# Performance work log

Hardware: AMD Instinct MI355X
Metric: run time of the kernel (lower is better)

Reference implementation:

```python
import jax, jax.numpy as jnp
import numpy as np

B, N, K = 2, 16384, 8
NH, HD, CH, KV_IN = 4, 32, 128, 128
EPS = 1e-5

def layer_norm(x, g, b):
    mu = x.mean(-1, keepdims=True)
    var = ((x - mu) ** 2).mean(-1, keepdims=True)
    return (x - mu) / jnp.sqrt(var + EPS) * g + b

def setup_inputs() -> dict:
    key = jax.random.key(0)
    ks = jax.random.split(key, 8)
    s = 0.02
    return {
        "query_in": jax.random.normal(ks[0], (B, N, CH), jnp.float32),
        "kv_in": jax.random.normal(ks[1], (B, N, K, KV_IN), jnp.float32),
        "w_kv": jax.random.normal(ks[2], (KV_IN, 2 * NH * HD), jnp.float32) * s,
        "w_q": jax.random.normal(ks[3], (CH, NH * HD), jnp.float32) * s,
        "w_mh": jax.random.normal(ks[4], (NH * HD, CH), jnp.float32) * s,
        "b_mh": jnp.zeros((CH,), jnp.float32),
        "w1": jax.random.normal(ks[5], (CH, CH), jnp.float32) * s,
        "b1": jnp.zeros((CH,), jnp.float32),
        "w2": jax.random.normal(ks[6], (CH, CH), jnp.float32) * s,
        "b2": jnp.zeros((CH,), jnp.float32),
        "ln1_g": jnp.ones((CH,), jnp.float32),
        "ln1_b": jnp.zeros((CH,), jnp.float32),
        "ln2_g": jnp.ones((CH,), jnp.float32),
        "ln2_b": jnp.zeros((CH,), jnp.float32),
    }

def reference(query_in, kv_in, w_kv, w_q, w_mh, b_mh, w1, b1, w2, b2,
              ln1_g, ln1_b, ln2_g, ln2_b):
    # q projection: [B,N,CH] -> [B,N,NH,HD]
    q = (query_in @ w_q).reshape(B, N, NH, HD)
    # kv projection: [B,N,K,KV_IN] -> [B,N,K,2,NH,HD]; chunk(2) on last dim
    kv = (kv_in @ w_kv).reshape(B, N, K, 2, NH, HD)
    k, v = kv[..., 0, :, :], kv[..., 1, :, :]  # each [B,N,K,NH,HD]
    # per-token local attention over its own K keys
    sim = jnp.einsum('bnhd,bnkhd->bnhk', q, k) / np.sqrt(HD).astype(np.float32)
    attn = jax.nn.softmax(sim, axis=-1)
    out = jnp.einsum('bnhk,bnkhd->bnhd', attn, v).reshape(B, N, NH * HD)
    out = out @ w_mh + b_mh
    res = layer_norm(out, ln1_g, ln1_b) + query_in
    # GELU MLP (torch nn.GELU default = exact erf form)
    mlp = jax.nn.gelu(res @ w1 + b1, approximate=False) @ w2 + b2
    return layer_norm(mlp + res, ln2_g, ln2_b)
```

## Files before the change

### kernel.cpp

```cpp
#include <hip/hip_runtime.h>
#include <hip/hip_fp16.h>

typedef _Float16 f16x8 __attribute__((ext_vector_type(8)));
typedef float f32x4 __attribute__((ext_vector_type(4)));
typedef unsigned int uint32;

#define LDW 136
#define TB  16

#define WAITLGKM() do { __builtin_amdgcn_s_waitcnt(0xC07F); __builtin_amdgcn_sched_barrier(0); } while(0)

#define BAR() do {                                          \
  asm volatile("s_waitcnt lgkmcnt(0)" ::: "memory");        \
  __builtin_amdgcn_sched_barrier(0);                        \
  __builtin_amdgcn_s_barrier();                             \
  __builtin_amdgcn_sched_barrier(0);                        \
} while (0)

union F16x8U { f16x8 v; __half2 h2[4]; uint2 u2[2]; uint4 u4; };

__device__ __forceinline__ uint32 pk2f(float a, float b) {
  __half2 h = __floats2half2_rn(a, b);
  return *reinterpret_cast<uint32*>(&h);
}
__device__ __forceinline__ float bcast(float v, int sl) {
  return __int_as_float(__builtin_amdgcn_readlane(__float_as_int(v), sl));
}
template <int CTRL, int RMASK = 0xF, int BMASK = 0xF>
__device__ __forceinline__ float dppmov(float v) {
  return __int_as_float(__builtin_amdgcn_update_dpp(
      0, __float_as_int(v), CTRL, RMASK, BMASK, true));
}
template <int PAT>
__device__ __forceinline__ float swzf(float v) {
  return __int_as_float(__builtin_amdgcn_ds_swizzle(__float_as_int(v), PAT));
}
__device__ __forceinline__ float wred_sum(float v) {
  v += dppmov<0x111>(v);
  v += dppmov<0x112>(v);
  v += dppmov<0x114>(v);
  v += dppmov<0x118>(v);
  v += dppmov<0x142, 0xA>(v);
  v += dppmov<0x143, 0xC>(v);
  return __int_as_float(__builtin_amdgcn_readlane(__float_as_int(v), 63));
}
__device__ __forceinline__ f16x8 ldsv8(const __half* p) {
  return *reinterpret_cast<const f16x8*>(p);
}
__device__ __forceinline__ f32x4 mfma16(f16x8 a, f16x8 b, f32x4 c) {
  return __builtin_amdgcn_mfma_f32_16x16x32_f16(a, b, c, 0, 0, 0);
}
__device__ __forceinline__ void stp(__half* base, int fr, int fq, int nt, f32x4 a) {
  uint2 u; u.x = pk2f(a[0], a[1]); u.y = pk2f(a[2], a[3]);
  *reinterpret_cast<uint2*>(&base[fr * LDW + nt * 16 + fq * 4]) = u;
}

#define OFF_WQ   0
#define OFF_WK2  16384
#define OFF_WV   36864
#define OFF_WMH  53248
#define OFF_W1   69632
#define OFF_W2   86016
#define WS_HALVES 102400

__global__ void prep_weights(const float* __restrict__ wq, const float* __restrict__ wkv,
                             const float* __restrict__ wmh, const float* __restrict__ w1,
                             const float* __restrict__ w2, __half* __restrict__ ws) {
  int idx = blockIdx.x * 256 + threadIdx.x;
  if (idx >= WS_HALVES) return;
  float v;
  if (idx < OFF_WK2) {
    int t = idx, c = t >> 7, k = t & 127;
    v = wq[k * 128 + c];
  } else if (idx < OFF_WV) {
    int t = idx - OFF_WK2;
    int d = t % 40, row = t / 40;
    int h = row >> 7, i = row & 127;
    v = (d < 32) ? wkv[i * 256 + h * 32 + d] : 0.f;
  } else if (idx < OFF_WMH) {
    int t = idx - OFF_WV, c = t >> 7, k = t & 127;
    v = wkv[k * 256 + 128 + c];
  } else if (idx < OFF_W1) {
    int t = idx - OFF_WMH, c = t >> 7, k = t & 127;
    v = wmh[k * 128 + c];
  } else if (idx < OFF_W2) {
    int t = idx - OFF_W1, c = t >> 7, k = t & 127;
    v = w1[k * 128 + c];
  } else {
    int t = idx - OFF_W2, c = t >> 7, k = t & 127;
    v = w2[k * 128 + c];
  }
  ws[idx] = __float2half_rn(v);
}

#define LOADB2(GOFF, NT0, NT1, BF) do {                                          \
  _Pragma("unroll")                                                              \
  for (int t_ = 0; t_ < 2; ++t_) {                                               \
    int nt_ = t_ ? (NT1) : (NT0);                                                \
    _Pragma("unroll")                                                            \
    for (int ks_ = 0; ks_ < 4; ++ks_)                                            \
      BF[t_][ks_] = *reinterpret_cast<const f16x8*>(                             \
          wsv + (GOFF) + (nt_*16 + fr)*128 + ks_*32 + fq*8);                     \
  } } while (0)

#define GEMM2(AT, BF, ACC0, ACC1) do {                                           \
  _Pragma("unroll")                                                              \
  for (int ks_ = 0; ks_ < 4; ++ks_) {                                            \
    f16x8 b_ = ldsv8(&(AT)[fr * LDW + ks_ * 32 + fq * 8]);                       \
    ACC0 = mfma16(BF[0][ks_], b_, ACC0);                                         \
    ACC1 = mfma16(BF[1][ks_], b_, ACC1);                                         \
  } } while (0)

__global__ void __launch_bounds__(256, 6) ca_mfma(
    const float* __restrict__ xq, const float* __restrict__ kvin,
    const __half* __restrict__ wsv,
    const float* __restrict__ bmh, const float* __restrict__ b1,
    const float* __restrict__ b2,
    const float* __restrict__ g1, const float* __restrict__ bb1,
    const float* __restrict__ g2, const float* __restrict__ bb2,
    float* __restrict__ outp)
{
  __shared__ __half QWC[64 * LDW];
  __shared__ __half UBUF[2 * TB * LDW];

  const int tid = threadIdx.x;
  const int wv = tid >> 6, lane = tid & 63;
  const int fr = lane & 15, fq = lane >> 4;
  const int tb = blockIdx.x * TB;
  const int ltb = wv * 4;

  __half* Xh = UBUF;
  __half* Qb = UBUF + 2176;
  __half* Ob = UBUF;
  __half* Yb   = QWC;
  __half* RESb = QWC + 16 * LDW;
  __half* Hb   = QWC + 32 * LDW;
  __half* Vb   = QWC + 48 * LDW;

  const f32x4 ZZ = {0.f, 0.f, 0.f, 0.f};

  float4 pre[4];
  {
    const float4* kv4 = reinterpret_cast<const float4*>(kvin + (size_t)(tb + ltb) * 1024);
    pre[0] = kv4[2 * lane];       pre[1] = kv4[2 * lane + 1];
    pre[2] = kv4[2 * lane + 128]; pre[3] = kv4[2 * lane + 129];
  }
  f16x8 bf[2][4];
  LOADB2(OFF_WQ, wv, 4 + wv, bf);

  {
    int tok = tid >> 4, ko = (tid & 15) * 8;
    const float4* s0 = reinterpret_cast<const float4*>(xq + (size_t)(tb + tok) * 128 + ko);
    float4 a = s0[0], b = s0[1];
    uint4 u; u.x = pk2f(a.x, a.y); u.y = pk2f(a.z, a.w);
    u.z = pk2f(b.x, b.y); u.w = pk2f(b.z, b.w);
    *reinterpret_cast<uint4*>(&Xh[tok * LDW + ko]) = u;
  }
  BAR();

  {
    f32x4 aA = ZZ, aB = ZZ;
    GEMM2(Xh, bf, aA, aB);
    stp(Qb, fr, fq, wv, aA);
    stp(Qb, fr, fq, 4 + wv, aB);
  }
  f16x8 bq[8];
#pragma unroll
  for (int nt = 0; nt < 8; ++nt)
    bq[nt] = *reinterpret_cast<const f16x8*>(
        wsv + OFF_WK2 + (wv * 128 + nt * 16 + fr) * 40 + fq * 8);
  BAR();

  {
    f16x8 aq = ldsv8(&Qb[fr * LDW + wv * 32 + fq * 8]);
#pragma unroll
    for (int nt = 0; nt < 8; ++nt) {
      f32x4 acc = mfma16(bq[nt], aq, ZZ);
      uint2 u; u.x = pk2f(acc[0], acc[1]); u.y = pk2f(acc[2], acc[3]);
      *reinterpret_cast<uint2*>(&QWC[(wv * 16 + fr) * LDW + nt * 16 + fq * 4]) = u;
    }
  }
  BAR();

  {
    const int kr = lane >> 4, i8 = (lane & 15) * 8;
    const int l2 = 2 * lane;
    const float SCALE = 0.17677669529663687f;
    __half* kvw = UBUF + wv * 1088;
#pragma unroll 1
    for (int lt = 0; lt < 4; ++lt) {
      const int ltok = ltb + lt;
      WAITLGKM();
      {
        uint4 u0, u1;
        u0.x = pk2f(pre[0].x, pre[0].y); u0.y = pk2f(pre[0].z, pre[0].w);
        u0.z = pk2f(pre[1].x, pre[1].y); u0.w = pk2f(pre[1].z, pre[1].w);
        u1.x = pk2f(pre[2].x, pre[2].y); u1.y = pk2f(pre[2].z, pre[2].w);
        u1.z = pk2f(pre[3].x, pre[3].y); u1.w = pk2f(pre[3].z, pre[3].w);
        *reinterpret_cast<uint4*>(&kvw[kr * LDW + i8]) = u0;
        *reinterpret_cast<uint4*>(&kvw[(4 + kr) * LDW + i8]) = u1;
      }
      if (lt < 3) {
        const float4* kv4 = reinterpret_cast<const float4*>(kvin + (size_t)(tb + ltok + 1) * 1024);
        pre[0] = kv4[2 * lane];       pre[1] = kv4[2 * lane + 1];
        pre[2] = kv4[2 * lane + 128]; pre[3] = kv4[2 * lane + 129];
      }
      WAITLGKM();
      f32x4 acc = ZZ;
#pragma unroll
      for (int ks = 0; ks < 4; ++ks) {
        f16x8 a_ = ldsv8(&QWC[((fr & 3) * 16 + ltok) * LDW + ks * 32 + fq * 8]);
        f16x8 b_ = ldsv8(&kvw[(fr & 7) * LDW + ks * 32 + fq * 8]);
        acc = mfma16(a_, b_, acc);
      }
      float at_[4];
#pragma unroll
      for (int r = 0; r < 4; ++r) {
        float s = acc[r] * SCALE;
        float mx = fmaxf(s, dppmov<0xB1>(s));
        mx = fmaxf(mx, dppmov<0x4E>(mx));
        mx = fmaxf(mx, swzf<0x101F>(mx));
        float e = __expf(s - mx);
        float dn = e + dppmov<0xB1>(e);
        dn += dppmov<0x4E>(dn);
        dn += swzf<0x101F>(dn);
        at_[r] = __fdividef(e, dn);
      }
      __half2 kvc[8];
#pragma unroll
      for (int k = 0; k < 8; ++k)
        kvc[k] = *reinterpret_cast<const __half2*>(&kvw[k * LDW + l2]);
#pragma unroll
      for (int h = 0; h < 4; ++h) {
        float c0 = 0.f, c1 = 0.f;
#pragma unroll
        for (int k = 0; k < 8; ++k) {
          float a = bcast(at_[h], k);
          float2 kf = __half22float2(kvc[k]);
          c0 = fmaf(a, kf.x, c0);
          c1 = fmaf(a, kf.y, c1);
        }
        *reinterpret_cast<__half2*>(&QWC[(h * 16 + ltok) * LDW + l2]) =
            __floats2half2_rn(c0, c1);
      }
    }
  }
  LOADB2(OFF_WV, wv, 4 + wv, bf);
  BAR();

  float2 xr[4];
#pragma unroll
  for (int lt = 0; lt < 4; ++lt) {
    int tok = tb + ltb + lt;
    xr[lt] = *reinterpret_cast<const float2*>(&xq[(size_t)tok * 128 + 2 * lane]);
  }
  {
    const int h1 = wv >> 1, h2 = 2 + (wv >> 1);
    f32x4 a1c = ZZ, a2c = ZZ;
#pragma unroll
    for (int ks = 0; ks < 4; ++ks) {
      f16x8 b1f = ldsv8(&QWC[(h1 * 16 + fr) * LDW + ks * 32 + fq * 8]);
      a1c = mfma16(bf[0][ks], b1f, a1c);
      f16x8 b2f = ldsv8(&QWC[(h2 * 16 + fr) * LDW + ks * 32 + fq * 8]);
      a2c = mfma16(bf[1][ks], b2f, a2c);
    }
    stp(Ob, fr, fq, wv, a1c);
    stp(Ob, fr, fq, 4 + wv, a2c);
  }
  LOADB2(OFF_WMH, wv, 4 + wv, bf);
  BAR();

  {
    f32x4 aA = ZZ, aB = ZZ;
    GEMM2(Ob, bf, aA, aB);
    stp(Yb, fr, fq, wv, aA);
    stp(Yb, fr, fq, 4 + wv, aB);
  }
  LOADB2(OFF_W1, wv, 4 + wv, bf);
  BAR();

  {
    const int l2 = 2 * lane;
    float2 bm = *reinterpret_cast<const float2*>(&bmh[l2]);
    float2 gg = *reinterpret_cast<const float2*>(&g1[l2]);
    float2 cc = *reinterpret_cast<const float2*>(&bb1[l2]);
#pragma unroll
    for (int lt = 0; lt < 4; ++lt) {
      int row = ltb + lt;
      float2 y = __half22float2(*reinterpret_cast<const __half2*>(&Yb[row * LDW + l2]));
      float v0 = y.x + bm.x, v1 = y.y + bm.y;
      float s = wred_sum(v0 + v1);
      float sq = wred_sum(v0 * v0 + v1 * v1);
      float mu = s * 0.0078125f;
      float var = sq * 0.0078125f - mu * mu;
      float rstd = rsqrtf(var + 1e-5f);
      float r0 = (v0 - mu) * rstd * gg.x + cc.x + xr[lt].x;
      float r1 = (v1 - mu) * rstd * gg.y + cc.y + xr[lt].y;
      *reinterpret_cast<__half2*>(&RESb[row * LDW + l2]) = __floats2half2_rn(r0, r1);
    }
  }
  BAR();

  {
    f32x4 aA = ZZ, aB = ZZ;
    GEMM2(RESb, bf, aA, aB);
    int c0 = wv * 16 + fq * 4, c1 = 64 + wv * 16 + fq * 4;
    float4 b1a = *reinterpret_cast<const float4*>(&b1[c0]);
    float4 b1b = *reinterpret_cast<const float4*>(&b1[c1]);
    uint2 ua, ub;
    float t0, t1;
    t0 = aA[0] + b1a.x; t0 = 0.5f * t0 * (1.f + erff(t0 * 0.70710678118654752f));
    t1 = aA[1] + b1a.y; t1 = 0.5f * t1 * (1.f + erff(t1 * 0.70710678118654752f));
    ua.x = pk2f(t0, t1);
    t0 = aA[2] + b1a.z; t0 = 0.5f * t0 * (1.f + erff(t0 * 0.70710678118654752f));
    t1 = aA[3] + b1a.w; t1 = 0.5f * t1 * (1.f + erff(t1 * 0.70710678118654752f));
    ua.y = pk2f(t0, t1);
    t0 = aB[0] + b1b.x; t0 = 0.5f * t0 * (1.f + erff(t0 * 0.70710678118654752f));
    t1 = aB[1] + b1b.y; t1 = 0.5f * t1 * (1.f + erff(t1 * 0.70710678118654752f));
    ub.x = pk2f(t0, t1);
    t0 = aB[2] + b1b.z; t0 = 0.5f * t0 * (1.f + erff(t0 * 0.70710678118654752f));
    t1 = aB[3] + b1b.w; t1 = 0.5f * t1 * (1.f + erff(t1 * 0.70710678118654752f));
    ub.y = pk2f(t0, t1);
    *reinterpret_cast<uint2*>(&Hb[fr * LDW + c0]) = ua;
    *reinterpret_cast<uint2*>(&Hb[fr * LDW + c1]) = ub;
  }
  LOADB2(OFF_W2, wv, 4 + wv, bf);
  BAR();

  {
    f32x4 aA = ZZ, aB = ZZ;
    GEMM2(Hb, bf, aA, aB);
    int c0 = wv * 16 + fq * 4, c1 = 64 + wv * 16 + fq * 4;
    float4 b2a = *reinterpret_cast<const float4*>(&b2[c0]);
    float4 b2b = *reinterpret_cast<const float4*>(&b2[c1]);
    F16x8U ra, rb;
    ra.u2[0] = *reinterpret_cast<const uint2*>(&RESb[fr * LDW + c0]);
    rb.u2[0] = *reinterpret_cast<const uint2*>(&RESb[fr * LDW + c1]);
    uint2 ua, ub;
    float2 p0 = __half22float2(ra.h2[0]), p1 = __half22float2(ra.h2[1]);
    ua.x = pk2f(aA[0] + b2a.x + p0.x, aA[1] + b2a.y + p0.y);
    ua.y = pk2f(aA[2] + b2a.z + p1.x, aA[3] + b2a.w + p1.y);
    float2 p2 = __half22float2(rb.h2[0]), p3 = __half22float2(rb.h2[1]);
    ub.x = pk2f(aB[0] + b2b.x + p2.x, aB[1] + b2b.y + p2.y);
    ub.y = pk2f(aB[2] + b2b.z + p3.x, aB[3] + b2b.w + p3.y);
    *reinterpret_cast<uint2*>(&Vb[fr * LDW + c0]) = ua;
    *reinterpret_cast<uint2*>(&Vb[fr * LDW + c1]) = ub;
  }
  BAR();

  {
    const int l2 = 2 * lane;
    float2 gg = *reinterpret_cast<const float2*>(&g2[l2]);
    float2 cc = *reinterpret_cast<const float2*>(&bb2[l2]);
#pragma unroll
    for (int lt = 0; lt < 4; ++lt) {
      int row = ltb + lt, tok = tb + row;
      float2 v = __half22float2(*reinterpret_cast<const __half2*>(&Vb[row * LDW + l2]));
      float s = wred_sum(v.x + v.y);
      float sq = wred_sum(v.x * v.x + v.y * v.y);
      float mu = s * 0.0078125f;
      float var = sq * 0.0078125f - mu * mu;
      float rstd = rsqrtf(var + 1e-5f);
      float2 o;
      o.x = (v.x - mu) * rstd * gg.x + cc.x;
      o.y = (v.y - mu) * rstd * gg.y + cc.y;
      *reinterpret_cast<float2*>(&outp[(size_t)tok * 128 + l2]) = o;
    }
  }
}

extern "C" void kernel_launch(void* const* d_in, const int* in_sizes, int n_in,
                              void* d_out, int out_size, void* d_ws, size_t ws_size,
                              hipStream_t stream) {
  const float* xq = (const float*)d_in[0];
  const float* kv = (const float*)d_in[1];
  const float* wkv = (const float*)d_in[2];
  const float* wq = (const float*)d_in[3];
  const float* wmh = (const float*)d_in[4];
  const float* bmh = (const float*)d_in[5];
  const float* w1 = (const float*)d_in[6];
  const float* b1 = (const float*)d_in[7];
  const float* w2 = (const float*)d_in[8];
  const float* b2 = (const float*)d_in[9];
  const float* g1 = (const float*)d_in[10];
  const float* bb1 = (const float*)d_in[11];
  const float* g2 = (const float*)d_in[12];
  const float* bb2 = (const float*)d_in[13];
  __half* ws = (__half*)d_ws;

  prep_weights<<<(WS_HALVES + 255) / 256, 256, 0, stream>>>(wq, wkv, wmh, w1, w2, ws);

  const int tokens = 32768;
  ca_mfma<<<tokens / TB, 256, 0, stream>>>(xq, kv, ws, bmh, b1, b2,
                                           g1, bb1, g2, bb2, (float*)d_out);
}
```

Before: 61.98 us.

## Fold Wq·Wk and Wv·Wmh into combined per-head weights to cut GEMM stages

Precomputes per-head products Wq_h·Wk_h^T and Wv_h·Wmh_h in the prep kernel. The main kernel then maps tokens directly to per-head query-in-kv space in one GEMM and applies a single 512-wide GEMM for value-projection plus output-projection. This removes one GEMM stage and one barrier in each path. In exchange the combined weights are larger (64K halves each, up from 16K), so more global/L2 weight traffic per block. It also changes fp16 rounding, since the products are formed in fp32 and then rounded once.

```diff
diff --git a/kernel.cpp b/kernel.cpp
--- a/kernel.cpp
+++ b/kernel.cpp
@@ -55,13 +55,11 @@
   *reinterpret_cast<uint2*>(&base[fr * LDW + nt * 16 + fq * 4]) = u;
 }
 
-#define OFF_WQ   0
-#define OFF_WK2  16384
-#define OFF_WV   36864
-#define OFF_WMH  53248
-#define OFF_W1   69632
-#define OFF_W2   86016
-#define WS_HALVES 102400
+#define OFF_WQK  0
+#define OFF_WVM  65536
+#define OFF_W1   131072
+#define OFF_W2   147456
+#define WS_HALVES 163840
 
 __global__ void prep_weights(const float* __restrict__ wq, const float* __restrict__ wkv,
                              const float* __restrict__ wmh, const float* __restrict__ w1,
@@ -69,20 +67,23 @@
   int idx = blockIdx.x * 256 + threadIdx.x;
   if (idx >= WS_HALVES) return;
   float v;
-  if (idx < OFF_WK2) {
-    int t = idx, c = t >> 7, k = t & 127;
-    v = wq[k * 128 + c];
-  } else if (idx < OFF_WV) {
-    int t = idx - OFF_WK2;
-    int d = t % 40, row = t / 40;
-    int h = row >> 7, i = row & 127;
-    v = (d < 32) ? wkv[i * 256 + h * 32 + d] : 0.f;
-  } else if (idx < OFF_WMH) {
-    int t = idx - OFF_WV, c = t >> 7, k = t & 127;
-    v = wkv[k * 256 + 128 + c];
+  if (idx < OFF_WVM) {
+    int h = idx >> 14, r = idx & 16383, i = r >> 7, c = r & 127;
+    const float* wqp = wq + c * 128 + h * 32;
+    const float* wkp = wkv + i * 256 + h * 32;
+    float acc = 0.f;
+#pragma unroll 8
+    for (int d = 0; d < 32; ++d) acc = fmaf(wqp[d], wkp[d], acc);
+    v = acc;
   } else if (idx < OFF_W1) {
-    int t = idx - OFF_WMH, c = t >> 7, k = t & 127;
-    v = wmh[k * 128 + c];
+    int t = idx - OFF_WVM;
+    int cp = t >> 9, k = t & 511, h = k >> 7, i = k & 127;
+    const float* wvp = wkv + i * 256 + 128 + h * 32;
+    const float* wmp = wmh + (h * 32) * 128 + cp;
+    float acc = 0.f;
+#pragma unroll 8
+    for (int d = 0; d < 32; ++d) acc = fmaf(wvp[d], wmp[d * 128], acc);
+    v = acc;
   } else if (idx < OFF_W2) {
     int t = idx - OFF_W1, c = t >> 7, k = t & 127;
     v = w1[k * 128 + c];
@@ -129,24 +130,13 @@
   const int tb = blockIdx.x * TB;
   const int ltb = wv * 4;
 
-  __half* Xh = UBUF;
-  __half* Qb = UBUF + 2176;
-  __half* Ob = UBUF;
-  __half* Yb   = QWC;
-  __half* RESb = QWC + 16 * LDW;
-  __half* Hb   = QWC + 32 * LDW;
-  __half* Vb   = QWC + 48 * LDW;
+  __half* Xh   = UBUF;
+  __half* Yb   = UBUF;
+  __half* RESb = UBUF + 16 * LDW;
+  __half* Hb   = QWC;
+  __half* Vb   = QWC + 16 * LDW;
 
   const f32x4 ZZ = {0.f, 0.f, 0.f, 0.f};
-
-  float4 pre[4];
-  {
-    const float4* kv4 = reinterpret_cast<const float4*>(kvin + (size_t)(tb + ltb) * 1024);
-    pre[0] = kv4[2 * lane];       pre[1] = kv4[2 * lane + 1];
-    pre[2] = kv4[2 * lane + 128]; pre[3] = kv4[2 * lane + 129];
-  }
-  f16x8 bf[2][4];
-  LOADB2(OFF_WQ, wv, 4 + wv, bf);
 
   {
     int tok = tid >> 4, ko = (tid & 15) * 8;
@@ -159,26 +149,33 @@
   BAR();
 
   {
-    f32x4 aA = ZZ, aB = ZZ;
-    GEMM2(Xh, bf, aA, aB);
-    stp(Qb, fr, fq, wv, aA);
-    stp(Qb, fr, fq, 4 + wv, aB);
-  }
-  f16x8 bq[8];
-#pragma unroll
-  for (int nt = 0; nt < 8; ++nt)
-    bq[nt] = *reinterpret_cast<const f16x8*>(
-        wsv + OFF_WK2 + (wv * 128 + nt * 16 + fr) * 40 + fq * 8);
-  BAR();
-
-  {
-    f16x8 aq = ldsv8(&Qb[fr * LDW + wv * 32 + fq * 8]);
-#pragma unroll
-    for (int nt = 0; nt < 8; ++nt) {
-      f32x4 acc = mfma16(bq[nt], aq, ZZ);
-      uint2 u; u.x = pk2f(acc[0], acc[1]); u.y = pk2f(acc[2], acc[3]);
-      *reinterpret_cast<uint2*>(&QWC[(wv * 16 + fr) * LDW + nt * 16 + fq * 4]) = u;
-    }
+    f16x8 bx[4];
+#pragma unroll
+    for (int ks = 0; ks < 4; ++ks) bx[ks] = ldsv8(&Xh[fr * LDW + ks * 32 + fq * 8]);
+    const __half* wqk = wsv + OFF_WQK + wv * 16384 + fr * 128 + fq * 8;
+#pragma unroll
+    for (int t = 0; t < 4; ++t) {
+      f16x8 a0[4], a1[4];
+#pragma unroll
+      for (int ks = 0; ks < 4; ++ks) {
+        a0[ks] = *reinterpret_cast<const f16x8*>(wqk + (2 * t) * 2048 + ks * 32);
+        a1[ks] = *reinterpret_cast<const f16x8*>(wqk + (2 * t + 1) * 2048 + ks * 32);
+      }
+      f32x4 q0 = ZZ, q1 = ZZ;
+#pragma unroll
+      for (int ks = 0; ks < 4; ++ks) {
+        q0 = mfma16(a0[ks], bx[ks], q0);
+        q1 = mfma16(a1[ks], bx[ks], q1);
+      }
+      stp(QWC + wv * 16 * LDW, fr, fq, 2 * t, q0);
+      stp(QWC + wv * 16 * LDW, fr, fq, 2 * t + 1, q1);
+    }
+  }
+  float4 pre[4];
+  {
+    const float4* kv4 = reinterpret_cast<const float4*>(kvin + (size_t)(tb + ltb) * 1024);
+    pre[0] = kv4[2 * lane];       pre[1] = kv4[2 * lane + 1];
+    pre[2] = kv4[2 * lane + 128]; pre[3] = kv4[2 * lane + 129];
   }
   BAR();
 
@@ -245,7 +242,6 @@
       }
     }
   }
-  LOADB2(OFF_WV, wv, 4 + wv, bf);
   BAR();
 
   float2 xr[4];
@@ -255,30 +251,31 @@
     xr[lt] = *reinterpret_cast<const float2*>(&xq[(size_t)tok * 128 + 2 * lane]);
   }
   {
-    const int h1 = wv >> 1, h2 = 2 + (wv >> 1);
-    f32x4 a1c = ZZ, a2c = ZZ;
-#pragma unroll
-    for (int ks = 0; ks < 4; ++ks) {
-      f16x8 b1f = ldsv8(&QWC[(h1 * 16 + fr) * LDW + ks * 32 + fq * 8]);
-      a1c = mfma16(bf[0][ks], b1f, a1c);
-      f16x8 b2f = ldsv8(&QWC[(h2 * 16 + fr) * LDW + ks * 32 + fq * 8]);
-      a2c = mfma16(bf[1][ks], b2f, a2c);
-    }
-    stp(Ob, fr, fq, wv, a1c);
-    stp(Ob, fr, fq, 4 + wv, a2c);
-  }
-  LOADB2(OFF_WMH, wv, 4 + wv, bf);
-  BAR();
-
-  {
-    f32x4 aA = ZZ, aB = ZZ;
-    GEMM2(Ob, bf, aA, aB);
-    stp(Yb, fr, fq, wv, aA);
-    stp(Yb, fr, fq, 4 + wv, aB);
-  }
-  LOADB2(OFF_W1, wv, 4 + wv, bf);
-  BAR();
-
+    const __half* wvmA = wsv + OFF_WVM + (size_t)(wv * 16 + fr) * 512 + fq * 8;
+    const __half* wvmB = wsv + OFF_WVM + (size_t)((4 + wv) * 16 + fr) * 512 + fq * 8;
+    f32x4 yA = ZZ, yB = ZZ;
+#pragma unroll
+    for (int t = 0; t < 4; ++t) {
+      f16x8 a0[4], a1[4], b[4];
+#pragma unroll
+      for (int j = 0; j < 4; ++j) {
+        int kk = 4 * t + j;
+        a0[j] = *reinterpret_cast<const f16x8*>(wvmA + kk * 32);
+        a1[j] = *reinterpret_cast<const f16x8*>(wvmB + kk * 32);
+        b[j]  = ldsv8(&QWC[(t * 16 + fr) * LDW + j * 32 + fq * 8]);
+      }
+#pragma unroll
+      for (int j = 0; j < 4; ++j) {
+        yA = mfma16(a0[j], b[j], yA);
+        yB = mfma16(a1[j], b[j], yB);
+      }
+    }
+    stp(Yb, fr, fq, wv, yA);
+    stp(Yb, fr, fq, 4 + wv, yB);
+  }
+  BAR();
+
+  f16x8 bf[2][4];
   {
     const int l2 = 2 * lane;
     float2 bm = *reinterpret_cast<const float2*>(&bmh[l2]);
@@ -299,6 +296,7 @@
       *reinterpret_cast<__half2*>(&RESb[row * LDW + l2]) = __floats2half2_rn(r0, r1);
     }
   }
+  LOADB2(OFF_W1, wv, 4 + wv, bf);
   BAR();
 
   {
```

Result: slower. 93.44 us (+50.8%).

## Process two 16-token sub-tiles per block to reuse loaded weight fragments

Applied to the files above, without the earlier changes.

Each block now handles 32 tokens as two 16-token sub-tiles, with the shared-memory buffers duplicated per sub-tile. Every weight fragment loaded into registers is applied to both sub-tiles, which halves global weight traffic and the number of barriers per token. The kv prefetch is doubled to two tokens per wave per step for more memory parallelism. In exchange, shared memory and register use per block roughly double and launch bounds drop to 3 blocks per CU, so occupancy falls.

```diff
diff --git a/kernel.cpp b/kernel.cpp
--- a/kernel.cpp
+++ b/kernel.cpp
@@ -6,7 +6,7 @@
 typedef unsigned int uint32;
 
 #define LDW 136
-#define TB  16
+#define TB  32
 
 #define WAITLGKM() do { __builtin_amdgcn_s_waitcnt(0xC07F); __builtin_amdgcn_sched_barrier(0); } while(0)
 
@@ -111,7 +111,7 @@
     ACC1 = mfma16(BF[1][ks_], b_, ACC1);                                         \
   } } while (0)
 
-__global__ void __launch_bounds__(256, 6) ca_mfma(
+__global__ void __launch_bounds__(256, 3) ca_mfma(
     const float* __restrict__ xq, const float* __restrict__ kvin,
     const __half* __restrict__ wsv,
     const float* __restrict__ bmh, const float* __restrict__ b1,
@@ -120,8 +120,8 @@
     const float* __restrict__ g2, const float* __restrict__ bb2,
     float* __restrict__ outp)
 {
-  __shared__ __half QWC[64 * LDW];
-  __shared__ __half UBUF[2 * TB * LDW];
+  __shared__ __half QWC[2 * 64 * LDW];
+  __shared__ __half UBUF[2 * 32 * LDW];
 
   const int tid = threadIdx.x;
   const int wv = tid >> 6, lane = tid & 63;
@@ -129,40 +129,42 @@
   const int tb = blockIdx.x * TB;
   const int ltb = wv * 4;
 
-  __half* Xh = UBUF;
-  __half* Qb = UBUF + 2176;
-  __half* Ob = UBUF;
-  __half* Yb   = QWC;
-  __half* RESb = QWC + 16 * LDW;
-  __half* Hb   = QWC + 32 * LDW;
-  __half* Vb   = QWC + 48 * LDW;
+  __half* const QWs[2] = {QWC, QWC + 64 * LDW};
+  __half* const Us[2]  = {UBUF, UBUF + 32 * LDW};
 
   const f32x4 ZZ = {0.f, 0.f, 0.f, 0.f};
 
-  float4 pre[4];
-  {
-    const float4* kv4 = reinterpret_cast<const float4*>(kvin + (size_t)(tb + ltb) * 1024);
-    pre[0] = kv4[2 * lane];       pre[1] = kv4[2 * lane + 1];
-    pre[2] = kv4[2 * lane + 128]; pre[3] = kv4[2 * lane + 129];
+  float4 pre[2][4];
+#pragma unroll
+  for (int st = 0; st < 2; ++st) {
+    const float4* kv4 = reinterpret_cast<const float4*>(
+        kvin + (size_t)(tb + st * 16 + ltb) * 1024);
+    pre[st][0] = kv4[2 * lane];       pre[st][1] = kv4[2 * lane + 1];
+    pre[st][2] = kv4[2 * lane + 128]; pre[st][3] = kv4[2 * lane + 129];
   }
   f16x8 bf[2][4];
   LOADB2(OFF_WQ, wv, 4 + wv, bf);
 
   {
     int tok = tid >> 4, ko = (tid & 15) * 8;
-    const float4* s0 = reinterpret_cast<const float4*>(xq + (size_t)(tb + tok) * 128 + ko);
-    float4 a = s0[0], b = s0[1];
-    uint4 u; u.x = pk2f(a.x, a.y); u.y = pk2f(a.z, a.w);
-    u.z = pk2f(b.x, b.y); u.w = pk2f(b.z, b.w);
-    *reinterpret_cast<uint4*>(&Xh[tok * LDW + ko]) = u;
-  }
-  BAR();
-
-  {
+#pragma unroll
+    for (int st = 0; st < 2; ++st) {
+      const float4* s0 = reinterpret_cast<const float4*>(
+          xq + (size_t)(tb + st * 16 + tok) * 128 + ko);
+      float4 a = s0[0], b = s0[1];
+      uint4 u; u.x = pk2f(a.x, a.y); u.y = pk2f(a.z, a.w);
+      u.z = pk2f(b.x, b.y); u.w = pk2f(b.z, b.w);
+      *reinterpret_cast<uint4*>(&Us[st][tok * LDW + ko]) = u;
+    }
+  }
+  BAR();
+
+#pragma unroll
+  for (int st = 0; st < 2; ++st) {
     f32x4 aA = ZZ, aB = ZZ;
-    GEMM2(Xh, bf, aA, aB);
-    stp(Qb, fr, fq, wv, aA);
-    stp(Qb, fr, fq, 4 + wv, aB);
+    GEMM2(Us[st], bf, aA, aB);
+    stp(Us[st] + 16 * LDW, fr, fq, wv, aA);
+    stp(Us[st] + 16 * LDW, fr, fq, 4 + wv, aB);
   }
   f16x8 bq[8];
 #pragma unroll
@@ -171,13 +173,14 @@
         wsv + OFF_WK2 + (wv * 128 + nt * 16 + fr) * 40 + fq * 8);
   BAR();
 
-  {
-    f16x8 aq = ldsv8(&Qb[fr * LDW + wv * 32 + fq * 8]);
+#pragma unroll
+  for (int st = 0; st < 2; ++st) {
+    f16x8 aq = ldsv8(&Us[st][16 * LDW + fr * LDW + wv * 32 + fq * 8]);
 #pragma unroll
     for (int nt = 0; nt < 8; ++nt) {
       f32x4 acc = mfma16(bq[nt], aq, ZZ);
       uint2 u; u.x = pk2f(acc[0], acc[1]); u.y = pk2f(acc[2], acc[3]);
-      *reinterpret_cast<uint2*>(&QWC[(wv * 16 + fr) * LDW + nt * 16 + fq * 4]) = u;
+      *reinterpret_cast<uint2*>(&QWs[st][(wv * 16 + fr) * LDW + nt * 16 + fq * 4]) = u;
     }
   }
   BAR();
@@ -186,95 +189,119 @@
     const int kr = lane >> 4, i8 = (lane & 15) * 8;
     const int l2 = 2 * lane;
     const float SCALE = 0.17677669529663687f;
-    __half* kvw = UBUF + wv * 1088;
 #pragma unroll 1
     for (int lt = 0; lt < 4; ++lt) {
       const int ltok = ltb + lt;
       WAITLGKM();
-      {
+#pragma unroll
+      for (int st = 0; st < 2; ++st) {
+        __half* kvw = Us[st] + wv * 1088;
         uint4 u0, u1;
-        u0.x = pk2f(pre[0].x, pre[0].y); u0.y = pk2f(pre[0].z, pre[0].w);
-        u0.z = pk2f(pre[1].x, pre[1].y); u0.w = pk2f(pre[1].z, pre[1].w);
-        u1.x = pk2f(pre[2].x, pre[2].y); u1.y = pk2f(pre[2].z, pre[2].w);
-        u1.z = pk2f(pre[3].x, pre[3].y); u1.w = pk2f(pre[3].z, pre[3].w);
+        u0.x = pk2f(pre[st][0].x, pre[st][0].y); u0.y = pk2f(pre[st][0].z, pre[st][0].w);
+        u0.z = pk2f(pre[st][1].x, pre[st][1].y); u0.w = pk2f(pre[st][1].z, pre[st][1].w);
+        u1.x = pk2f(pre[st][2].x, pre[st][2].y); u1.y = pk2f(pre[st][2].z, pre[st][2].w);
+        u1.z = pk2f(pre[st][3].x, pre[st][3].y); u1.w = pk2f(pre[st][3].z, pre[st][3].w);
         *reinterpret_cast<uint4*>(&kvw[kr * LDW + i8]) = u0;
         *reinterpret_cast<uint4*>(&kvw[(4 + kr) * LDW + i8]) = u1;
       }
       if (lt < 3) {
-        const float4* kv4 = reinterpret_cast<const float4*>(kvin + (size_t)(tb + ltok + 1) * 1024);
-        pre[0] = kv4[2 * lane];       pre[1] = kv4[2 * lane + 1];
-        pre[2] = kv4[2 * lane + 128]; pre[3] = kv4[2 * lane + 129];
+#pragma unroll
+        for (int st = 0; st < 2; ++st) {
+          const float4* kv4 = reinterpret_cast<const float4*>(
+              kvin + (size_t)(tb + st * 16 + ltok + 1) * 1024);
+          pre[st][0] = kv4[2 * lane];       pre[st][1] = kv4[2 * lane + 1];
+          pre[st][2] = kv4[2 * lane + 128]; pre[st][3] = kv4[2 * lane + 129];
+        }
       }
       WAITLGKM();
-      f32x4 acc = ZZ;
+      f32x4 acc[2];
+#pragma unroll
+      for (int st = 0; st < 2; ++st) {
+        __half* kvw = Us[st] + wv * 1088;
+        f32x4 a = ZZ;
+#pragma unroll
+        for (int ks = 0; ks < 4; ++ks) {
+          f16x8 a_ = ldsv8(&QWs[st][((fr & 3) * 16 + ltok) * LDW + ks * 32 + fq * 8]);
+          f16x8 b_ = ldsv8(&kvw[(fr & 7) * LDW + ks * 32 + fq * 8]);
+          a = mfma16(a_, b_, a);
+        }
+        acc[st] = a;
+      }
+      float at_[2][4];
+#pragma unroll
+      for (int st = 0; st < 2; ++st) {
+#pragma unroll
+        for (int r = 0; r < 4; ++r) {
+          float s = acc[st][r] * SCALE;
+          float mx = fmaxf(s, dppmov<0xB1>(s));
+          mx = fmaxf(mx, dppmov<0x4E>(mx));
+          mx = fmaxf(mx, swzf<0x101F>(mx));
+          float e = __expf(s - mx);
+          float dn = e + dppmov<0xB1>(e);
+          dn += dppmov<0x4E>(dn);
+          dn += swzf<0x101F>(dn);
+          at_[st][r] = __fdividef(e, dn);
+        }
+      }
+#pragma unroll
+      for (int st = 0; st < 2; ++st) {
+        __half* kvw = Us[st] + wv * 1088;
+        __half2 kvc[8];
+#pragma unroll
+        for (int k = 0; k < 8; ++k)
+          kvc[k] = *reinterpret_cast<const __half2*>(&kvw[k * LDW + l2]);
+#pragma unroll
+        for (int h = 0; h < 4; ++h) {
+          float c0 = 0.f, c1 = 0.f;
+#pragma unroll
+          for (int k = 0; k < 8; ++k) {
+            float a = bcast(at_[st][h], k);
+            float2 kf = __half22float2(kvc[k]);
+            c0 = fmaf(a, kf.x, c0);
+            c1 = fmaf(a, kf.y, c1);
+          }
+          *reinterpret_cast<__half2*>(&QWs[st][(h * 16 + ltok) * LDW + l2]) =
+              __floats2half2_rn(c0, c1);
+        }
+      }
+    }
+  }
+  LOADB2(OFF_WV, wv, 4 + wv, bf);
+  BAR();
+
+  float2 xr[2][4];
+#pragma unroll
+  for (int st = 0; st < 2; ++st)
+#pragma unroll
+    for (int lt = 0; lt < 4; ++lt) {
+      int tok = tb + st * 16 + ltb + lt;
+      xr[st][lt] = *reinterpret_cast<const float2*>(&xq[(size_t)tok * 128 + 2 * lane]);
+    }
+  {
+    const int h1 = wv >> 1, h2 = 2 + (wv >> 1);
+#pragma unroll
+    for (int st = 0; st < 2; ++st) {
+      f32x4 a1c = ZZ, a2c = ZZ;
 #pragma unroll
       for (int ks = 0; ks < 4; ++ks) {
-        f16x8 a_ = ldsv8(&QWC[((fr & 3) * 16 + ltok) * LDW + ks * 32 + fq * 8]);
-        f16x8 b_ = ldsv8(&kvw[(fr & 7) * LDW + ks * 32 + fq * 8]);
-        acc = mfma16(a_, b_, acc);
-      }
-      float at_[4];
-#pragma unroll
-      for (int r = 0; r < 4; ++r) {
-        float s = acc[r] * SCALE;
-        float mx = fmaxf(s, dppmov<0xB1>(s));
-        mx = fmaxf(mx, dppmov<0x4E>(mx));
-        mx = fmaxf(mx, swzf<0x101F>(mx));
-        float e = __expf(s - mx);
-        float dn = e + dppmov<0xB1>(e);
-        dn += dppmov<0x4E>(dn);
-        dn += swzf<0x101F>(dn);
-        at_[r] = __fdividef(e, dn);
-      }
-      __half2 kvc[8];
-#pragma unroll
-      for (int k = 0; k < 8; ++k)
-        kvc[k] = *reinterpret_cast<const __half2*>(&kvw[k * LDW + l2]);
-#pragma unroll
-      for (int h = 0; h < 4; ++h) {
-        float c0 = 0.f, c1 = 0.f;
-#pragma unroll
-        for (int k = 0; k < 8; ++k) {
-          float a = bcast(at_[h], k);
-          float2 kf = __half22float2(kvc[k]);
-          c0 = fmaf(a, kf.x, c0);
-          c1 = fmaf(a, kf.y, c1);
-        }
-        *reinterpret_cast<__half2*>(&QWC[(h * 16 + ltok) * LDW + l2]) =
-            __floats2half2_rn(c0, c1);
-      }
-    }
-  }
-  LOADB2(OFF_WV, wv, 4 + wv, bf);
-  BAR();
-
-  float2 xr[4];
-#pragma unroll
-  for (int lt = 0; lt < 4; ++lt) {
-    int tok = tb + ltb + lt;
-    xr[lt] = *reinterpret_cast<const float2*>(&xq[(size_t)tok * 128 + 2 * lane]);
-  }
-  {
-    const int h1 = wv >> 1, h2 = 2 + (wv >> 1);
-    f32x4 a1c = ZZ, a2c = ZZ;
-#pragma unroll
-    for (int ks = 0; ks < 4; ++ks) {
-      f16x8 b1f = ldsv8(&QWC[(h1 * 16 + fr) * LDW + ks * 32 + fq * 8]);
-      a1c = mfma16(bf[0][ks], b1f, a1c);
-      f16x8 b2f = ldsv8(&QWC[(h2 * 16 + fr) * LDW + ks * 32 + fq * 8]);
-      a2c = mfma16(bf[1][ks], b2f, a2c);
-    }
-    stp(Ob, fr, fq, wv, a1c);
-    stp(Ob, fr, fq, 4 + wv, a2c);
+        f16x8 b1f = ldsv8(&QWs[st][(h1 * 16 + fr) * LDW + ks * 32 + fq * 8]);
+        a1c = mfma16(bf[0][ks], b1f, a1c);
+        f16x8 b2f = ldsv8(&QWs[st][(h2 * 16 + fr) * LDW + ks * 32 + fq * 8]);
+        a2c = mfma16(bf[1][ks], b2f, a2c);
+      }
+      stp(Us[st], fr, fq, wv, a1c);
+      stp(Us[st], fr, fq, 4 + wv, a2c);
+    }
   }
   LOADB2(OFF_WMH, wv, 4 + wv, bf);
   BAR();
 
-  {
+#pragma unroll
+  for (int st = 0; st < 2; ++st) {
     f32x4 aA = ZZ, aB = ZZ;
-    GEMM2(Ob, bf, aA, aB);
-    stp(Yb, fr, fq, wv, aA);
-    stp(Yb, fr, fq, 4 + wv, aB);
+    GEMM2(Us[st], bf, aA, aB);
+    stp(QWs[st], fr, fq, wv, aA);
+    stp(QWs[st], fr, fq, 4 + wv, aB);
   }
   LOADB2(OFF_W1, wv, 4 + wv, bf);
   BAR();
@@ -285,66 +312,76 @@
     float2 gg = *reinterpret_cast<const float2*>(&g1[l2]);
     float2 cc = *reinterpret_cast<const float2*>(&bb1[l2]);
 #pragma unroll
-    for (int lt = 0; lt < 4; ++lt) {
-      int row = ltb + lt;
-      float2 y = __half22float2(*reinterpret_cast<const __half2*>(&Yb[row * LDW + l2]));
-      float v0 = y.x + bm.x, v1 = y.y + bm.y;
-      float s = wred_sum(v0 + v1);
-      float sq = wred_sum(v0 * v0 + v1 * v1);
-      float mu = s * 0.0078125f;
-      float var = sq * 0.0078125f - mu * mu;
-      float rstd = rsqrtf(var + 1e-5f);
-      float r0 = (v0 - mu) * rstd * gg.x + cc.x + xr[lt].x;
-      float r1 = (v1 - mu) * rstd * gg.y + cc.y + xr[lt].y;
-      *reinterpret_cast<__half2*>(&RESb[row * LDW + l2]) = __floats2half2_rn(r0, r1);
-    }
-  }
-  BAR();
-
-  {
-    f32x4 aA = ZZ, aB = ZZ;
-    GEMM2(RESb, bf, aA, aB);
+    for (int st = 0; st < 2; ++st)
+#pragma unroll
+      for (int lt = 0; lt < 4; ++lt) {
+        int row = ltb + lt;
+        float2 y = __half22float2(
+            *reinterpret_cast<const __half2*>(&QWs[st][row * LDW + l2]));
+        float v0 = y.x + bm.x, v1 = y.y + bm.y;
+        float s = wred_sum(v0 + v1);
+        float sq = wred_sum(v0 * v0 + v1 * v1);
+        float mu = s * 0.0078125f;
+        float var = sq * 0.0078125f - mu * mu;
+        float rstd = rsqrtf(var + 1e-5f);
+        float r0 = (v0 - mu) * rstd * gg.x + cc.x + xr[st][lt].x;
+        float r1 = (v1 - mu) * rstd * gg.y + cc.y + xr[st][lt].y;
+        *reinterpret_cast<__half2*>(&QWs[st][(16 + row) * LDW + l2]) =
+            __floats2half2_rn(r0, r1);
+      }
+  }
+  BAR();
+
+  {
     int c0 = wv * 16 + fq * 4, c1 = 64 + wv * 16 + fq * 4;
     float4 b1a = *reinterpret_cast<const float4*>(&b1[c0]);
     float4 b1b = *reinterpret_cast<const float4*>(&b1[c1]);
-    uint2 ua, ub;
-    float t0, t1;
-    t0 = aA[0] + b1a.x; t0 = 0.5f * t0 * (1.f + erff(t0 * 0.70710678118654752f));
-    t1 = aA[1] + b1a.y; t1 = 0.5f * t1 * (1.f + erff(t1 * 0.70710678118654752f));
-    ua.x = pk2f(t0, t1);
-    t0 = aA[2] + b1a.z; t0 = 0.5f * t0 * (1.f + erff(t0 * 0.70710678118654752f));
-    t1 = aA[3] + b1a.w; t1 = 0.5f * t1 * (1.f + erff(t1 * 0.70710678118654752f));
-    ua.y = pk2f(t0, t1);
-    t0 = aB[0] + b1b.x; t0 = 0.5f * t0 * (1.f + erff(t0 * 0.70710678118654752f));
-    t1 = aB[1] + b1b.y; t1 = 0.5f * t1 * (1.f + erff(t1 * 0.70710678118654752f));
-    ub.x = pk2f(t0, t1);
-    t0 = aB[2] + b1b.z; t0 = 0.5f * t0 * (1.f + erff(t0 * 0.70710678118654752f));
-    t1 = aB[3] + b1b.w; t1 = 0.5f * t1 * (1.f + erff(t1 * 0.70710678118654752f));
-    ub.y = pk2f(t0, t1);
-    *reinterpret_cast<uint2*>(&Hb[fr * LDW + c0]) = ua;
-    *reinterpret_cast<uint2*>(&Hb[fr * LDW + c1]) = ub;
+#pragma unroll
+    for (int st = 0; st < 2; ++st) {
+      f32x4 aA = ZZ, aB = ZZ;
+      GEMM2(QWs[st] + 16 * LDW, bf, aA, aB);
+      uint2 ua, ub;
+      float t0, t1;
+      t0 = aA[0] + b1a.x; t0 = 0.5f * t0 * (1.f + erff(t0 * 0.70710678118654752f));
+      t1 = aA[1] + b1a.y; t1 = 0.5f * t1 * (1.f + erff(t1 * 0.70710678118654752f));
+      ua.x = pk2f(t0, t1);
+      t0 = aA[2] + b1a.z; t0 = 0.5f * t0 * (1.f + erff(t0 * 0.70710678118654752f));
+      t1 = aA[3] + b1a.w; t1 = 0.5f * t1 * (1.f + erff(t1 * 0.70710678118654752f));
+      ua.y = pk2f(t0, t1);
+      t0 = aB[0] + b1b.x; t0 = 0.5f * t0 * (1.f + erff(t0 * 0.70710678118654752f));
+      t1 = aB[1] + b1b.y; t1 = 0.5f * t1 * (1.f + erff(t1 * 0.70710678118654752f));
+      ub.x = pk2f(t0, t1);
+      t0 = aB[2] + b1b.z; t0 = 0.5f * t0 * (1.f + erff(t0 * 0.70710678118654752f));
+      t1 = aB[3] + b1b.w; t1 = 0.5f * t1 * (1.f + erff(t1 * 0.70710678118654752f));
+      ub.y = pk2f(t0, t1);
+      *reinterpret_cast<uint2*>(&QWs[st][(32 + fr) * LDW + c0]) = ua;
+      *reinterpret_cast<uint2*>(&QWs[st][(32 + fr) * LDW + c1]) = ub;
+    }
   }
   LOADB2(OFF_W2, wv, 4 + wv, bf);
   BAR();
 
   {
-    f32x4 aA = ZZ, aB = ZZ;
-    GEMM2(Hb, bf, aA, aB);
     int c0 = wv * 16 + fq * 4, c1 = 64 + wv * 16 + fq * 4;
     float4 b2a = *reinterpret_cast<const float4*>(&b2[c0]);
     float4 b2b = *reinterpret_cast<const float4*>(&b2[c1]);
-    F16x8U ra, rb;
-    ra.u2[0] = *reinterpret_cast<const uint2*>(&RESb[fr * LDW + c0]);
-    rb.u2[0] = *reinterpret_cast<const uint2*>(&RESb[fr * LDW + c1]);
-    uint2 ua, ub;
-    float2 p0 = __half22float2(ra.h2[0]), p1 = __half22float2(ra.h2[1]);
-    ua.x = pk2f(aA[0] + b2a.x + p0.x, aA[1] + b2a.y + p0.y);
-    ua.y = pk2f(aA[2] + b2a.z + p1.x, aA[3] + b2a.w + p1.y);
-    float2 p2 = __half22float2(rb.h2[0]), p3 = __half22float2(rb.h2[1]);
-    ub.x = pk2f(aB[0] + b2b.x + p2.x, aB[1] + b2b.y + p2.y);
-    ub.y = pk2f(aB[2] + b2b.z + p3.x, aB[3] + b2b.w + p3.y);
-    *reinterpret_cast<uint2*>(&Vb[fr * LDW + c0]) = ua;
-    *reinterpret_cast<uint2*>(&Vb[fr * LDW + c1]) = ub;
+#pragma unroll
+    for (int st = 0; st < 2; ++st) {
+      f32x4 aA = ZZ, aB = ZZ;
+      GEMM2(QWs[st] + 32 * LDW, bf, aA, aB);
+      F16x8U ra, rb;
+      ra.u2[0] = *reinterpret_cast<const uint2*>(&QWs[st][(16 + fr) * LDW + c0]);
+      rb.u2[0] = *reinterpret_cast<const uint2*>(&QWs[st][(16 + fr) * LDW + c1]);
+      uint2 ua, ub;
+      float2 p0 = __half22float2(ra.h2[0]), p1 = __half22float2(ra.h2[1]);
+      ua.x = pk2f(aA[0] + b2a.x + p0.x, aA[1] + b2a.y + p0.y);
+      ua.y = pk2f(aA[2] + b2a.z + p1.x, aA[3] + b2a.w + p1.y);
+      float2 p2 = __half22float2(rb.h2[0]), p3 = __half22float2(rb.h2[1]);
+      ub.x = pk2f(aB[0] + b2b.x + p2.x, aB[1] + b2b.y + p2.y);
+      ub.y = pk2f(aB[2] + b2b.z + p3.x, aB[3] + b2b.w + p3.y);
+      *reinterpret_cast<uint2*>(&QWs[st][(48 + fr) * LDW + c0]) = ua;
+      *reinterpret_cast<uint2*>(&QWs[st][(48 + fr) * LDW + c1]) = ub;
+    }
   }
   BAR();
 
@@ -353,19 +390,22 @@
     float2 gg = *reinterpret_cast<const float2*>(&g2[l2]);
     float2 cc = *reinterpret_cast<const float2*>(&bb2[l2]);
 #pragma unroll
-    for (int lt = 0; lt < 4; ++lt) {
-      int row = ltb + lt, tok = tb + row;
-      float2 v = __half22float2(*reinterpret_cast<const __half2*>(&Vb[row * LDW + l2]));
-      float s = wred_sum(v.x + v.y);
-      float sq = wred_sum(v.x * v.x + v.y * v.y);
-      float mu = s * 0.0078125f;
-      float var = sq * 0.0078125f - mu * mu;
-      float rstd = rsqrtf(var + 1e-5f);
-      float2 o;
-      o.x = (v.x - mu) * rstd * gg.x + cc.x;
-      o.y = (v.y - mu) * rstd * gg.y + cc.y;
-      *reinterpret_cast<float2*>(&outp[(size_t)tok * 128 + l2]) = o;
-    }
+    for (int st = 0; st < 2; ++st)
+#pragma unroll
+      for (int lt = 0; lt < 4; ++lt) {
+        int row = ltb + lt, tok = tb + st * 16 + row;
+        float2 v = __half22float2(
+            *reinterpret_cast<const __half2*>(&QWs[st][(48 + row) * LDW + l2]));
+        float s = wred_sum(v.x + v.y);
+        float sq = wred_sum(v.x * v.x + v.y * v.y);
+        float mu = s * 0.0078125f;
+        float var = sq * 0.0078125f - mu * mu;
+        float rstd = rsqrtf(var + 1e-5f);
+        float2 o;
+        o.x = (v.x - mu) * rstd * gg.x + cc.x;
+        o.y = (v.y - mu) * rstd * gg.y + cc.y;
+        *reinterpret_cast<float2*>(&outp[(size_t)tok * 128 + l2]) = o;
+      }
   }
 }
 
```

Result: faster. 54.43 us (-12.2%).
